# Optimization experiments

Hardware: AMD Instinct MI355X
Metric: run time of the kernel (lower is better)

Reference implementation:

```python
import jax, jax.numpy as jnp
import numpy as np

B, L, H, NH, NB = 16, 200, 128, 2, 2
ITEMS, SPAN = 50000, 256
NEG = -2.0**32 + 1.0  # mask value used by the torch module


def _ln(x, g, b, eps=1e-8):
    m = jnp.mean(x, axis=-1, keepdims=True)
    v = jnp.mean((x - m) ** 2, axis=-1, keepdims=True)
    return (x - m) / jnp.sqrt(v + eps) * g + b


def setup_inputs() -> dict:
    key = jax.random.key(0)
    ks = jax.random.split(key, 20)
    p = lambda k, s: (jax.random.normal(k, s, jnp.float32) * 0.02)
    item_emb = p(ks[0], (ITEMS + 1, H)).at[0].set(0.0)  # padding_idx=0
    return {
        "user_ids": jax.random.randint(ks[1], (B,), 0, 10000),
        "log_seqs": jax.random.randint(ks[2], (B, L), 0, ITEMS),
        "time_matrices": jax.random.randint(ks[3], (B, L, L), 0, SPAN),
        "pos_seqs": jax.random.randint(ks[4], (B, L), 0, ITEMS),
        "neg_seqs": jax.random.randint(ks[5], (B, L), 0, ITEMS),
        "item_emb": item_emb,
        "pos_K_emb": p(ks[6], (L, H)),
        "pos_V_emb": p(ks[7], (L, H)),
        "time_K_emb": p(ks[8], (SPAN + 1, H)),
        "time_V_emb": p(ks[9], (SPAN + 1, H)),
        "Wq": p(ks[10], (NB, H, H)), "bq": jnp.zeros((NB, H)),
        "Wk": p(ks[11], (NB, H, H)), "bk": jnp.zeros((NB, H)),
        "Wv": p(ks[12], (NB, H, H)), "bv": jnp.zeros((NB, H)),
        "ln1_g": jnp.ones((NB, H)), "ln1_b": jnp.zeros((NB, H)),
        "W1": p(ks[13], (NB, H, H)), "b1": jnp.zeros((NB, H)),
        "W2": p(ks[14], (NB, H, H)), "b2": jnp.zeros((NB, H)),
        "ln2_g": jnp.ones((NB, H)), "ln2_b": jnp.zeros((NB, H)),
        "lnf_g": jnp.ones((H,)), "lnf_b": jnp.zeros((H,)),
    }


def reference(user_ids, log_seqs, time_matrices, pos_seqs, neg_seqs,
              item_emb, pos_K_emb, pos_V_emb, time_K_emb, time_V_emb,
              Wq, bq, Wk, bk, Wv, bv, ln1_g, ln1_b,
              W1, b1, W2, b2, ln2_g, ln2_b, lnf_g, lnf_b):
    d = H // NH
    pad = (log_seqs == 0)                    # (B,L) timeline mask
    keep = (~pad)[..., None].astype(jnp.float32)

    seqs = item_emb[log_seqs] * jnp.sqrt(jnp.float32(H))
    seqs = seqs * keep
    posK = pos_K_emb.reshape(L, NH, d)       # same for every batch element
    posV = pos_V_emb.reshape(L, NH, d)
    tmK = time_K_emb[time_matrices].reshape(B, L, L, NH, d)  # (B,L,L,h,d)
    tmV = time_V_emb[time_matrices].reshape(B, L, L, NH, d)
    causal = ~jnp.tril(jnp.ones((L, L), dtype=bool))          # True = masked
    mask = pad[:, None, :, None] | causal[None, None, :, :]   # (B,1,L,L) row-mask | causal

    for i in range(NB):
        Q = (seqs @ Wq[i].T + bq[i]).reshape(B, L, NH, d)
        K = (seqs @ Wk[i].T + bk[i]).reshape(B, L, NH, d)
        V = (seqs @ Wv[i].T + bv[i]).reshape(B, L, NH, d)
        aw = jnp.einsum('bqhd,bkhd->bhqk', Q, K)
        aw = aw + jnp.einsum('bqhd,khd->bhqk', Q, posK)
        aw = aw + jnp.einsum('bqkhd,bqhd->bhqk', tmK, Q)
        aw = aw / jnp.sqrt(jnp.float32(d))
        aw = jnp.where(mask, NEG, aw)
        A = jax.nn.softmax(aw, axis=-1)                        # (B,h,L,L)
        out = jnp.einsum('bhqk,bkhd->bqhd', A, V)
        out = out + jnp.einsum('bhqk,khd->bqhd', A, posV)
        out = out + jnp.einsum('bhqk,bqkhd->bqhd', A, tmV)
        out = out.reshape(B, L, H)
        seqs = _ln(seqs + out, ln1_g[i], ln1_b[i])
        ffn = jax.nn.relu(seqs @ W1[i].T + b1[i]) @ W2[i].T + b2[i]
        seqs = _ln(seqs + ffn, ln2_g[i], ln2_b[i])
        seqs = seqs * keep

    log_feats = _ln(seqs, lnf_g, lnf_b)
    pos_logits = jnp.sum(log_feats * item_emb[pos_seqs], axis=-1)  # (B,L)
    neg_logits = jnp.sum(log_feats * item_emb[neg_seqs], axis=-1)
    return jnp.stack([pos_logits, neg_logits])  # (2,B,L)
```

## Files before the change

kernel.cpp:

```cpp
#include <hip/hip_runtime.h>
#include <hip/hip_bf16.h>
#include <math.h>

#define BB 16
#define LL 200
#define HH 128
#define DD 64
#define QT2 8
#define NQT2 25
#define NEGF -4294967295.0f
#define SQRTH 11.313708498984761f

__global__ __launch_bounds__(512) void k_qkv_proj(float* __restrict__ seqs,
    const int* __restrict__ log_seqs, const float* __restrict__ item_emb, int do_embed,
    const float* __restrict__ Wq, const float* __restrict__ bq,
    const float* __restrict__ Wk, const float* __restrict__ bk,
    const float* __restrict__ Wv, const float* __restrict__ bv,
    const float* __restrict__ posK, const float* __restrict__ posV,
    const float* __restrict__ timeK,
    float* __restrict__ Q, float* __restrict__ Kp, float* __restrict__ Vp,
    float* __restrict__ projK) {
    __shared__ float s_lds[16][HH];
    __shared__ float TK[32][132];
    int r0g = blockIdx.x * 16;
    int t = threadIdx.x;
    if (do_embed) {
        int r = t >> 5, d4 = t & 31;
        int id = log_seqs[r0g + r];
        float4 v = make_float4(0.f, 0.f, 0.f, 0.f);
        if (id != 0) {
            v = ((const float4*)(item_emb + id * HH))[d4];
            v.x *= SQRTH; v.y *= SQRTH; v.z *= SQRTH; v.w *= SQRTH;
        }
        *(float4*)&s_lds[r][d4 * 4] = v;
        ((float4*)(seqs + r0g * HH))[t] = v;
    } else {
        ((float4*)s_lds)[t] = ((const float4*)(seqs + r0g * HH))[t];
    }
    __syncthreads();
    int c = t & 127, rg = t >> 7;
    float aq[4] = {0.f, 0.f, 0.f, 0.f};
    float ak[4] = {0.f, 0.f, 0.f, 0.f};
    float av[4] = {0.f, 0.f, 0.f, 0.f};
    const float4* wq4 = (const float4*)(Wq + c * HH);
    const float4* wk4 = (const float4*)(Wk + c * HH);
    const float4* wv4 = (const float4*)(Wv + c * HH);
#pragma unroll 4
    for (int k4 = 0; k4 < HH / 4; ++k4) {
        float4 wq = wq4[k4], wk = wk4[k4], wv = wv4[k4];
#pragma unroll
        for (int r = 0; r < 4; ++r) {
            float4 s = *(const float4*)&s_lds[rg * 4 + r][k4 * 4];
            aq[r] += s.x * wq.x + s.y * wq.y + s.z * wq.z + s.w * wq.w;
            ak[r] += s.x * wk.x + s.y * wk.y + s.z * wk.z + s.w * wk.w;
            av[r] += s.x * wv.x + s.y * wv.y + s.z * wv.z + s.w * wv.w;
        }
    }
    __syncthreads();
#pragma unroll
    for (int r = 0; r < 4; ++r) {
        int row = r0g + rg * 4 + r;
        int l = row % LL;
        float qv = aq[r] + bq[c];
        Q[row * HH + c]  = qv;
        s_lds[rg * 4 + r][c] = qv;
        Kp[row * HH + c] = ak[r] + bk[c] + posK[l * HH + c];
        Vp[row * HH + c] = av[r] + bv[c] + posV[l * HH + c];
    }
    int tq = t >> 5, ttl = t & 31;
    int row = r0g + tq;
    int brow = row / LL, lrow = row - brow * LL;
    for (int ch = 0; ch < 9; ++ch) {
        int base = ch * 32;
        __syncthreads();
        for (int x = t; x < 32 * 32; x += 512) {
            int i = x >> 5, d4 = x & 31;
            int tt = base + i;
            if (tt < 257)
                *(float4*)&TK[i][d4 * 4] = ((const float4*)(timeK + tt * HH))[d4];
        }
        __syncthreads();
        int tt = base + ttl;
        if (tt < 257) {
#pragma unroll
            for (int h = 0; h < 2; ++h) {
                float acc = 0.f;
#pragma unroll
                for (int d4 = 0; d4 < 16; ++d4) {
                    float4 qv = *(const float4*)&s_lds[tq][h * DD + d4 * 4];
                    float4 kv = *(const float4*)&TK[ttl][h * DD + d4 * 4];
                    acc += qv.x * kv.x + qv.y * kv.y + qv.z * kv.z + qv.w * kv.w;
                }
                projK[((brow * 2 + h) * LL + lrow) * 257 + tt] = acc;
            }
        }
    }
}

__global__ __launch_bounds__(256) void k_attn(
    const float* __restrict__ Q, const float* __restrict__ Kp, const float* __restrict__ Vp,
    const float* __restrict__ projK, const float* __restrict__ timeV,
    const int* __restrict__ tm, const int* __restrict__ log_seqs,
    float* __restrict__ attnout) {
    int bh = blockIdx.x / NQT2, qt = blockIdx.x % NQT2;
    int b = bh >> 1, h = bh & 1;
    int qlo = qt * QT2;
    __shared__ float K_s[32][68];
    __shared__ float smemW[457 * 12];
    __shared__ float proj_T[257][9];
    __shared__ unsigned long long pm64[4];
    __shared__ int s_allmask;
#define WT(i, j) smemW[(i) * 12 + (j)]
    int t = threadIdx.x;
    int tq = t >> 5, lane = t & 31, g = tq;
    int q = qlo + tq;
    int qhi = qlo + QT2 - 1;

    {
        bool keep = (t < LL) && (log_seqs[b * LL + t] != 0);
        unsigned long long ball = __ballot(keep);
        if ((t & 63) == 0) pm64[t >> 6] = ball;
    }
    if (t == 0) s_allmask = 0;
    for (int x = t; x < 200 * 12; x += 256) smemW[x] = NEGF;
    for (int x = 200 * 12 + t; x < 457 * 12; x += 256) smemW[x] = 0.f;
    {
        const float* pbase = projK + (bh * LL + qlo) * 257;
        for (int x = t; x < 8 * 257; x += 256) {
            int qq = x / 257, tt = x - qq * 257;
            proj_T[tt][qq] = pbase[x];
        }
    }
    float4 qreg[16];
    {
        const float4* qp = (const float4*)(Q + (b * LL + q) * HH + h * DD);
#pragma unroll
        for (int d4 = 0; d4 < 16; ++d4) qreg[d4] = qp[d4];
    }
    const int* tmrow = tm + (b * LL + q) * LL;
    __syncthreads();

    int nkc = (qhi >> 5) + 1;
    for (int kc = 0; kc < nkc; ++kc) {
        int kbase = kc * 32;
        for (int x = t; x < 512; x += 256) {
            int i = x >> 4, d4 = x & 15;
            int k = kbase + i;
            if (k < LL)
                *(float4*)&K_s[i][d4 * 4] =
                    ((const float4*)(Kp + (b * LL + k) * HH + h * DD))[d4];
        }
        __syncthreads();
        int k = kbase + lane;
        if (k <= q && ((pm64[k >> 6] >> (k & 63)) & 1ull)) {
            float acc = 0.f;
#pragma unroll
            for (int d4 = 0; d4 < 16; ++d4) {
                float4 kv = *(const float4*)&K_s[lane][d4 * 4];
                acc += qreg[d4].x * kv.x + qreg[d4].y * kv.y +
                       qreg[d4].z * kv.z + qreg[d4].w * kv.w;
            }
            WT(k, tq) = (acc + proj_T[tmrow[k]][tq]) * 0.125f;
        }
        __syncthreads();
    }

    float mx = -INFINITY;
    for (int k = lane; k < LL; k += 32) mx = fmaxf(mx, WT(k, tq));
    mx = fmaxf(mx, __shfl_xor(mx, 1, 64));
    mx = fmaxf(mx, __shfl_xor(mx, 2, 64));
    mx = fmaxf(mx, __shfl_xor(mx, 4, 64));
    mx = fmaxf(mx, __shfl_xor(mx, 8, 64));
    mx = fmaxf(mx, __shfl_xor(mx, 16, 64));
    bool allmask = (mx == NEGF);
    float sum = 0.f;
    for (int k = lane; k < LL; k += 32) {
        float e = __expf(WT(k, tq) - mx);
        WT(k, tq) = e;
        sum += e;
    }
    sum += __shfl_xor(sum, 1, 64);
    sum += __shfl_xor(sum, 2, 64);
    sum += __shfl_xor(sum, 4, 64);
    sum += __shfl_xor(sum, 8, 64);
    sum += __shfl_xor(sum, 16, 64);
    float inv = 1.0f / sum;
    int klim = allmask ? LL : (q + 1);
    if (allmask && lane == 0) s_allmask = 1;
    for (int k = lane; k < LL; k += 32) {
        float p = WT(k, tq) * inv;
        WT(k, tq) = p;
        if (k < klim) atomicAdd(&WT(200 + tmrow[k], tq), p);
    }
    __syncthreads();

    int kmax = s_allmask ? LL : (qhi + 1);
    float a00=0.f,a01=0.f,a10=0.f,a11=0.f,a20=0.f,a21=0.f,a30=0.f,a31=0.f;
    float a40=0.f,a41=0.f,a50=0.f,a51=0.f,a60=0.f,a61=0.f,a70=0.f,a71=0.f;
#define PV_STEP(WROW, SRCPTR)                                            \
    {                                                                    \
        const float* wr = &WROW;                                         \
        float4 w0 = *(const float4*)wr;                                  \
        float4 w1 = *(const float4*)(wr + 4);                            \
        float2 vv = *(const float2*)(SRCPTR);                            \
        a00 += w0.x * vv.x; a01 += w0.x * vv.y;                          \
        a10 += w0.y * vv.x; a11 += w0.y * vv.y;                          \
        a20 += w0.z * vv.x; a21 += w0.z * vv.y;                          \
        a30 += w0.w * vv.x; a31 += w0.w * vv.y;                          \
        a40 += w1.x * vv.x; a41 += w1.x * vv.y;                          \
        a50 += w1.y * vv.x; a51 += w1.y * vv.y;                          \
        a60 += w1.z * vv.x; a61 += w1.z * vv.y;                          \
        a70 += w1.w * vv.x; a71 += w1.w * vv.y;                          \
    }
    for (int i = g; i < kmax; i += 8)
        PV_STEP(WT(i, 0), Vp + (b * LL + i) * HH + h * DD + lane * 2);
    for (int i = g; i < 257; i += 8)
        PV_STEP(WT(200 + i, 0), timeV + i * HH + h * DD + lane * 2);
#undef PV_STEP
    __syncthreads();
    float* part = smemW;
    part[g * 512 + 0 * 64 + lane * 2] = a00; part[g * 512 + 0 * 64 + lane * 2 + 1] = a01;
    part[g * 512 + 1 * 64 + lane * 2] = a10; part[g * 512 + 1 * 64 + lane * 2 + 1] = a11;
    part[g * 512 + 2 * 64 + lane * 2] = a20; part[g * 512 + 2 * 64 + lane * 2 + 1] = a21;
    part[g * 512 + 3 * 64 + lane * 2] = a30; part[g * 512 + 3 * 64 + lane * 2 + 1] = a31;
    part[g * 512 + 4 * 64 + lane * 2] = a40; part[g * 512 + 4 * 64 + lane * 2 + 1] = a41;
    part[g * 512 + 5 * 64 + lane * 2] = a50; part[g * 512 + 5 * 64 + lane * 2 + 1] = a51;
    part[g * 512 + 6 * 64 + lane * 2] = a60; part[g * 512 + 6 * 64 + lane * 2 + 1] = a61;
    part[g * 512 + 7 * 64 + lane * 2] = a70; part[g * 512 + 7 * 64 + lane * 2 + 1] = a71;
    __syncthreads();
    {
        float ox = 0.f, oy = 0.f;
#pragma unroll
        for (int gg = 0; gg < 8; ++gg) {
            ox += part[gg * 512 + tq * 64 + lane * 2];
            oy += part[gg * 512 + tq * 64 + lane * 2 + 1];
        }
        *(float2*)(attnout + (b * LL + q) * HH + h * DD + lane * 2) =
            make_float2(ox, oy);
    }
#undef WT
}

__global__ __launch_bounds__(512) void k_ffn_full(
    float* __restrict__ seqs, const float* __restrict__ AO,
    const float* __restrict__ g1, const float* __restrict__ be1,
    const float* __restrict__ W1, const float* __restrict__ b1,
    const float* __restrict__ W2, const float* __restrict__ b2,
    const float* __restrict__ g2, const float* __restrict__ be2,
    const int* __restrict__ log_seqs, int do_final,
    const float* __restrict__ lnf_g, const float* __restrict__ lnf_b,
    const float* __restrict__ item_emb,
    const int* __restrict__ pos_seqs, const int* __restrict__ neg_seqs,
    float* __restrict__ out) {
    __shared__ float s_lds[16][HH];
    __shared__ float h_lds[16][HH];
    int r0g = blockIdx.x * 16;
    int t = threadIdx.x;
    {
        float4 a = ((const float4*)(seqs + r0g * HH))[t];
        float4 o = ((const float4*)(AO + r0g * HH))[t];
        a.x += o.x; a.y += o.y; a.z += o.z; a.w += o.w;
        ((float4*)s_lds)[t] = a;
    }
    __syncthreads();
    int w = t >> 6, lane = t & 63;
    int lrow = w * 2 + (lane >> 5), cl = lane & 31;
    {
        float sm = 0.f;
#pragma unroll
        for (int j = 0; j < 4; ++j) sm += s_lds[lrow][cl + 32 * j];
        sm += __shfl_xor(sm, 1, 64);
        sm += __shfl_xor(sm, 2, 64);
        sm += __shfl_xor(sm, 4, 64);
        sm += __shfl_xor(sm, 8, 64);
        sm += __shfl_xor(sm, 16, 64);
        float mean = sm * (1.0f / HH);
        float vr = 0.f;
#pragma unroll
        for (int j = 0; j < 4; ++j) {
            float d = s_lds[lrow][cl + 32 * j] - mean;
            vr += d * d;
        }
        vr += __shfl_xor(vr, 1, 64);
        vr += __shfl_xor(vr, 2, 64);
        vr += __shfl_xor(vr, 4, 64);
        vr += __shfl_xor(vr, 8, 64);
        vr += __shfl_xor(vr, 16, 64);
        float rstd = rsqrtf(vr * (1.0f / HH) + 1e-8f);
#pragma unroll
        for (int j = 0; j < 4; ++j) {
            int c = cl + 32 * j;
            s_lds[lrow][c] = (s_lds[lrow][c] - mean) * rstd * g1[c] + be1[c];
        }
    }
    __syncthreads();
    int c = t & 127, rg = t >> 7;
    float acc[4] = {0.f, 0.f, 0.f, 0.f};
    const float4* w14 = (const float4*)(W1 + c * HH);
#pragma unroll 4
    for (int k4 = 0; k4 < HH / 4; ++k4) {
        float4 ww = w14[k4];
#pragma unroll
        for (int r = 0; r < 4; ++r) {
            float4 s = *(const float4*)&s_lds[rg * 4 + r][k4 * 4];
            acc[r] += s.x * ww.x + s.y * ww.y + s.z * ww.z + s.w * ww.w;
        }
    }
#pragma unroll
    for (int r = 0; r < 4; ++r) h_lds[rg * 4 + r][c] = fmaxf(acc[r] + b1[c], 0.f);
    __syncthreads();
#pragma unroll
    for (int r = 0; r < 4; ++r) acc[r] = 0.f;
    const float4* w24 = (const float4*)(W2 + c * HH);
#pragma unroll 4
    for (int k4 = 0; k4 < HH / 4; ++k4) {
        float4 ww = w24[k4];
#pragma unroll
        for (int r = 0; r < 4; ++r) {
            float4 s = *(const float4*)&h_lds[rg * 4 + r][k4 * 4];
            acc[r] += s.x * ww.x + s.y * ww.y + s.z * ww.z + s.w * ww.w;
        }
    }
    __syncthreads();
#pragma unroll
    for (int r = 0; r < 4; ++r)
        h_lds[rg * 4 + r][c] = s_lds[rg * 4 + r][c] + acc[r] + b2[c];
    __syncthreads();
    {
        float sm = 0.f;
#pragma unroll
        for (int j = 0; j < 4; ++j) sm += h_lds[lrow][cl + 32 * j];
        sm += __shfl_xor(sm, 1, 64);
        sm += __shfl_xor(sm, 2, 64);
        sm += __shfl_xor(sm, 4, 64);
        sm += __shfl_xor(sm, 8, 64);
        sm += __shfl_xor(sm, 16, 64);
        float mean = sm * (1.0f / HH);
        float vr = 0.f;
#pragma unroll
        for (int j = 0; j < 4; ++j) {
            float d = h_lds[lrow][cl + 32 * j] - mean;
            vr += d * d;
        }
        vr += __shfl_xor(vr, 1, 64);
        vr += __shfl_xor(vr, 2, 64);
        vr += __shfl_xor(vr, 4, 64);
        vr += __shfl_xor(vr, 8, 64);
        vr += __shfl_xor(vr, 16, 64);
        float rstd = rsqrtf(vr * (1.0f / HH) + 1e-8f);
        int row = r0g + lrow;
        float keep = (log_seqs[row] != 0) ? 1.0f : 0.0f;
        float y2[4];
#pragma unroll
        for (int j = 0; j < 4; ++j) {
            int cc = cl + 32 * j;
            y2[j] = ((h_lds[lrow][cc] - mean) * rstd * g2[cc] + be2[cc]) * keep;
        }
        if (!do_final) {
#pragma unroll
            for (int j = 0; j < 4; ++j)
                seqs[row * HH + cl + 32 * j] = y2[j];
        } else {
            float sm2 = y2[0] + y2[1] + y2[2] + y2[3];
            sm2 += __shfl_xor(sm2, 1, 64);
            sm2 += __shfl_xor(sm2, 2, 64);
            sm2 += __shfl_xor(sm2, 4, 64);
            sm2 += __shfl_xor(sm2, 8, 64);
            sm2 += __shfl_xor(sm2, 16, 64);
            float mean2 = sm2 * (1.0f / HH);
            float vr2 = 0.f;
#pragma unroll
            for (int j = 0; j < 4; ++j) {
                float d = y2[j] - mean2;
                vr2 += d * d;
            }
            vr2 += __shfl_xor(vr2, 1, 64);
            vr2 += __shfl_xor(vr2, 2, 64);
            vr2 += __shfl_xor(vr2, 4, 64);
            vr2 += __shfl_xor(vr2, 8, 64);
            vr2 += __shfl_xor(vr2, 16, 64);
            float rstd2 = rsqrtf(vr2 * (1.0f / HH) + 1e-8f);
            int pid = pos_seqs[row];
            int nid = neg_seqs[row];
            float pp = 0.f, nn = 0.f;
#pragma unroll
            for (int j = 0; j < 4; ++j) {
                int cc = cl + 32 * j;
                float lf = (y2[j] - mean2) * rstd2 * lnf_g[cc] + lnf_b[cc];
                pp += lf * item_emb[pid * HH + cc];
                nn += lf * item_emb[nid * HH + cc];
            }
            pp += __shfl_xor(pp, 1, 64);
            pp += __shfl_xor(pp, 2, 64);
            pp += __shfl_xor(pp, 4, 64);
            pp += __shfl_xor(pp, 8, 64);
            pp += __shfl_xor(pp, 16, 64);
            nn += __shfl_xor(nn, 1, 64);
            nn += __shfl_xor(nn, 2, 64);
            nn += __shfl_xor(nn, 4, 64);
            nn += __shfl_xor(nn, 8, 64);
            nn += __shfl_xor(nn, 16, 64);
            if (cl == 0) {
                out[row] = pp;
                out[BB * LL + row] = nn;
            }
        }
    }
}

extern "C" void kernel_launch(void* const* d_in, const int* in_sizes, int n_in,
                              void* d_out, int out_size, void* d_ws, size_t ws_size,
                              hipStream_t stream) {
    const int* log_seqs = (const int*)d_in[1];
    const int* tm       = (const int*)d_in[2];
    const int* pos_seqs = (const int*)d_in[3];
    const int* neg_seqs = (const int*)d_in[4];
    const float* item_emb = (const float*)d_in[5];
    const float* posK   = (const float*)d_in[6];
    const float* posV   = (const float*)d_in[7];
    const float* timeK  = (const float*)d_in[8];
    const float* timeV  = (const float*)d_in[9];
    const float* Wq = (const float*)d_in[10];
    const float* bq = (const float*)d_in[11];
    const float* Wk = (const float*)d_in[12];
    const float* bk = (const float*)d_in[13];
    const float* Wv = (const float*)d_in[14];
    const float* bv = (const float*)d_in[15];
    const float* ln1_g = (const float*)d_in[16];
    const float* ln1_b = (const float*)d_in[17];
    const float* W1 = (const float*)d_in[18];
    const float* b1 = (const float*)d_in[19];
    const float* W2 = (const float*)d_in[20];
    const float* b2 = (const float*)d_in[21];
    const float* ln2_g = (const float*)d_in[22];
    const float* ln2_b = (const float*)d_in[23];
    const float* lnf_g = (const float*)d_in[24];
    const float* lnf_b = (const float*)d_in[25];

    float* ws    = (float*)d_ws;
    float* seqs  = ws;
    float* Qb    = seqs + 409600;
    float* Kpb   = Qb + 409600;
    float* Vpb   = Kpb + 409600;
    float* AO    = Vpb + 409600;
    float* projK = AO + 409600;

    for (int i = 0; i < 2; ++i) {
        k_qkv_proj<<<BB * LL / 16, 512, 0, stream>>>(seqs, log_seqs, item_emb,
            (i == 0) ? 1 : 0,
            Wq + i * HH * HH, bq + i * HH,
            Wk + i * HH * HH, bk + i * HH,
            Wv + i * HH * HH, bv + i * HH,
            posK, posV, timeK, Qb, Kpb, Vpb, projK);
        k_attn<<<32 * NQT2, 256, 0, stream>>>(Qb, Kpb, Vpb, projK, timeV,
                                              tm, log_seqs, AO);
        k_ffn_full<<<BB * LL / 16, 512, 0, stream>>>(seqs, AO,
            ln1_g + i * HH, ln1_b + i * HH,
            W1 + i * HH * HH, b1 + i * HH,
            W2 + i * HH * HH, b2 + i * HH,
            ln2_g + i * HH, ln2_b + i * HH, log_seqs,
            (i == 1) ? 1 : 0, lnf_g, lnf_b, item_emb,
            pos_seqs, neg_seqs, (float*)d_out);
    }
}
```

Measured before the change: 191.4 us.

## Split Q·timeK projection into separate per-head kernel and read projK directly in attention

Moves the Q-times-timeK projection out of the QKV kernel into its own kernel, gridded by (batch, head, 16-query tile), which loads only the head's 64-wide slice of timeK. The attention kernel stops staging an 8x257 proj_T tile in shared memory and gathers projK from global memory by time index instead. The aim is to shorten the QKV kernel, give the projection more parallelism, and free LDS in attention. In exchange it adds a kernel launch per block and uncoalesced global gathers in the attention inner loop.

Measured after the change: 197.8 us. 1.03x slower.

```diff
diff --git a/kernel.cpp b/kernel.cpp
--- a/kernel.cpp
+++ b/kernel.cpp
@@ -11,17 +11,14 @@
 #define NEGF -4294967295.0f
 #define SQRTH 11.313708498984761f
 
-__global__ __launch_bounds__(512) void k_qkv_proj(float* __restrict__ seqs,
+__global__ __launch_bounds__(512) void k_qkv(float* __restrict__ seqs,
     const int* __restrict__ log_seqs, const float* __restrict__ item_emb, int do_embed,
     const float* __restrict__ Wq, const float* __restrict__ bq,
     const float* __restrict__ Wk, const float* __restrict__ bk,
     const float* __restrict__ Wv, const float* __restrict__ bv,
     const float* __restrict__ posK, const float* __restrict__ posV,
-    const float* __restrict__ timeK,
-    float* __restrict__ Q, float* __restrict__ Kp, float* __restrict__ Vp,
-    float* __restrict__ projK) {
+    float* __restrict__ Q, float* __restrict__ Kp, float* __restrict__ Vp) {
     __shared__ float s_lds[16][HH];
-    __shared__ float TK[32][132];
     int r0g = blockIdx.x * 16;
     int t = threadIdx.x;
     if (do_embed) {
@@ -56,42 +53,57 @@
             av[r] += s.x * wv.x + s.y * wv.y + s.z * wv.z + s.w * wv.w;
         }
     }
-    __syncthreads();
 #pragma unroll
     for (int r = 0; r < 4; ++r) {
         int row = r0g + rg * 4 + r;
         int l = row % LL;
-        float qv = aq[r] + bq[c];
-        Q[row * HH + c]  = qv;
-        s_lds[rg * 4 + r][c] = qv;
+        Q[row * HH + c]  = aq[r] + bq[c];
         Kp[row * HH + c] = ak[r] + bk[c] + posK[l * HH + c];
         Vp[row * HH + c] = av[r] + bv[c] + posV[l * HH + c];
     }
-    int tq = t >> 5, ttl = t & 31;
-    int row = r0g + tq;
-    int brow = row / LL, lrow = row - brow * LL;
-    for (int ch = 0; ch < 9; ++ch) {
-        int base = ch * 32;
+}
+
+__global__ __launch_bounds__(256) void k_proj(const float* __restrict__ Q,
+    const float* __restrict__ timeK, float* __restrict__ projK) {
+    int bh = blockIdx.x / 13, qt = blockIdx.x % 13;
+    int b = bh >> 1, h = bh & 1;
+    int qlo = qt * 16;
+    __shared__ float Qs[16][68];
+    __shared__ float TK[32][68];
+    int t = threadIdx.x;
+    {
+        int r = t >> 4, d4 = t & 15;
+        int q = qlo + r;
+        float4 v = make_float4(0.f, 0.f, 0.f, 0.f);
+        if (q < LL) v = ((const float4*)(Q + (b * LL + q) * HH + h * DD))[d4];
+        *(float4*)&Qs[r][d4 * 4] = v;
+    }
+    int tq = t >> 4, ttl = t & 15;
+    int q = qlo + tq;
+    for (int c = 0; c < 9; ++c) {
+        int base = c * 32;
         __syncthreads();
-        for (int x = t; x < 32 * 32; x += 512) {
-            int i = x >> 5, d4 = x & 31;
+        for (int x = t; x < 512; x += 256) {
+            int i = x >> 4, d4 = x & 15;
             int tt = base + i;
             if (tt < 257)
-                *(float4*)&TK[i][d4 * 4] = ((const float4*)(timeK + tt * HH))[d4];
+                *(float4*)&TK[i][d4 * 4] =
+                    ((const float4*)(timeK + tt * HH + h * DD))[d4];
         }
         __syncthreads();
-        int tt = base + ttl;
-        if (tt < 257) {
-#pragma unroll
-            for (int h = 0; h < 2; ++h) {
+#pragma unroll
+        for (int j = 0; j < 2; ++j) {
+            int ti = ttl + 16 * j;
+            int tt = base + ti;
+            if (tt < 257 && q < LL) {
                 float acc = 0.f;
 #pragma unroll
                 for (int d4 = 0; d4 < 16; ++d4) {
-                    float4 qv = *(const float4*)&s_lds[tq][h * DD + d4 * 4];
-                    float4 kv = *(const float4*)&TK[ttl][h * DD + d4 * 4];
+                    float4 qv = *(const float4*)&Qs[tq][d4 * 4];
+                    float4 kv = *(const float4*)&TK[ti][d4 * 4];
                     acc += qv.x * kv.x + qv.y * kv.y + qv.z * kv.z + qv.w * kv.w;
                 }
-                projK[((brow * 2 + h) * LL + lrow) * 257 + tt] = acc;
+                projK[(bh * LL + q) * 257 + tt] = acc;
             }
         }
     }
@@ -107,7 +119,6 @@
     int qlo = qt * QT2;
     __shared__ float K_s[32][68];
     __shared__ float smemW[457 * 12];
-    __shared__ float proj_T[257][9];
     __shared__ unsigned long long pm64[4];
     __shared__ int s_allmask;
 #define WT(i, j) smemW[(i) * 12 + (j)]
@@ -124,13 +135,6 @@
     if (t == 0) s_allmask = 0;
     for (int x = t; x < 200 * 12; x += 256) smemW[x] = NEGF;
     for (int x = 200 * 12 + t; x < 457 * 12; x += 256) smemW[x] = 0.f;
-    {
-        const float* pbase = projK + (bh * LL + qlo) * 257;
-        for (int x = t; x < 8 * 257; x += 256) {
-            int qq = x / 257, tt = x - qq * 257;
-            proj_T[tt][qq] = pbase[x];
-        }
-    }
     float4 qreg[16];
     {
         const float4* qp = (const float4*)(Q + (b * LL + q) * HH + h * DD);
@@ -138,6 +142,7 @@
         for (int d4 = 0; d4 < 16; ++d4) qreg[d4] = qp[d4];
     }
     const int* tmrow = tm + (b * LL + q) * LL;
+    const float* projrow = projK + (bh * LL + q) * 257;
     __syncthreads();
 
     int nkc = (qhi >> 5) + 1;
@@ -160,7 +165,7 @@
                 acc += qreg[d4].x * kv.x + qreg[d4].y * kv.y +
                        qreg[d4].z * kv.z + qreg[d4].w * kv.w;
             }
-            WT(k, tq) = (acc + proj_T[tmrow[k]][tq]) * 0.125f;
+            WT(k, tq) = (acc + projrow[tmrow[k]]) * 0.125f;
         }
         __syncthreads();
     }
@@ -446,12 +451,13 @@
     float* projK = AO + 409600;
 
     for (int i = 0; i < 2; ++i) {
-        k_qkv_proj<<<BB * LL / 16, 512, 0, stream>>>(seqs, log_seqs, item_emb,
+        k_qkv<<<BB * LL / 16, 512, 0, stream>>>(seqs, log_seqs, item_emb,
             (i == 0) ? 1 : 0,
             Wq + i * HH * HH, bq + i * HH,
             Wk + i * HH * HH, bk + i * HH,
             Wv + i * HH * HH, bv + i * HH,
-            posK, posV, timeK, Qb, Kpb, Vpb, projK);
+            posK, posV, Qb, Kpb, Vpb);
+        k_proj<<<32 * 13, 256, 0, stream>>>(Qb, timeK, projK);
         k_attn<<<32 * NQT2, 256, 0, stream>>>(Qb, Kpb, Vpb, projK, timeV,
                                               tm, log_seqs, AO);
         k_ffn_full<<<BB * LL / 16, 512, 0, stream>>>(seqs, AO,
```
